# Performance work log

Hardware: AMD Instinct MI355X
Metric: run time of the kernel (lower is better)

## Reference

```python
import jax, jax.numpy as jnp
import numpy as np

NEG_INF = -10000.0  # matches the original max_val init
EPS = 1e-8          # torch.nn.CosineSimilarity default eps


def setup_inputs() -> dict:
    key = jax.random.key(0)
    k1, k2, k3 = jax.random.split(key, 3)
    B, S, H = 32, 1024, 1024
    seq = jax.random.normal(k1, (B, S, H), dtype=jnp.float32)
    # sep0 = index of first [SEP] (end of question), sep1 = end of passage
    sep0 = jax.random.randint(k2, (B, 1), 32, 128)
    sep1 = jax.random.randint(k3, (B, 1), 768, S)
    idxs = jnp.concatenate([sep0, sep1], axis=1).astype(jnp.int64)
    return {"sequence_outputs": seq, "idxs": idxs, "max_ans_len": 32}


def reference(sequence_outputs, idxs, max_ans_len):
    # sequence_outputs: [B, S, H] float; idxs: [B, 2] int (sep0, sep1)
    B, S, H = sequence_outputs.shape
    L = max_ans_len
    sep0 = idxs[:, 0]
    sep1 = idxs[:, 1]

    # question_cat_repr = cat(seq[1], seq[sep0-1]); cos over the 2H concat
    # decomposes as (h_i.q1 + h_j.q2) / (sqrt(|h_i|^2+|h_j|^2) * |q|)
    q1 = sequence_outputs[:, 1, :]                                   # [B, H]
    q2 = jnp.take_along_axis(
        sequence_outputs, (sep0 - 1)[:, None, None], axis=1)[:, 0, :]  # [B, H]
    qn2 = jnp.sum(q1 * q1, -1) + jnp.sum(q2 * q2, -1)                # [B]

    d1 = jnp.einsum('bsh,bh->bs', sequence_outputs, q1)             # [B, S]
    d2 = jnp.einsum('bsh,bh->bs', sequence_outputs, q2)             # [B, S]
    n2 = jnp.sum(sequence_outputs * sequence_outputs, -1)           # [B, S]

    # banded window: for start i, ends j = i + l, l in [0, L)
    i = jnp.arange(S)[:, None]                                      # [S, 1]
    l = jnp.arange(L)[None, :]                                      # [1, L]
    j = jnp.minimum(i + l, S - 1)                                   # [S, L]
    d2w = d2[:, j]                                                  # [B, S, L]
    n2w = n2[:, j]                                                  # [B, S, L]

    denom = jnp.maximum(
        jnp.sqrt((n2[:, :, None] + n2w) * qn2[:, None, None]), EPS)
    sim = (d1[:, :, None] + d2w) / denom                            # [B, S, L]

    # valid ends: j = i + l < min(sep1, i + L); (i+l >= S implies invalid too)
    valid_j = (i + l)[None, :, :] < sep1[:, None, None]
    sim = jnp.where(valid_j, sim, NEG_INF)

    max_vals = jnp.max(sim, axis=-1)                                # [B, S]
    end_idx = jnp.arange(S)[None, :] + jnp.argmax(sim, axis=-1)     # [B, S]

    # valid starts: sep0 + 1 <= i < sep1
    pos = jnp.arange(S)[None, :]
    valid_i = (pos > sep0[:, None]) & (pos < sep1[:, None])
    max_vals = jnp.where(valid_i, max_vals, NEG_INF)
    end_idx = jnp.where(valid_i, end_idx, -1)
    return max_vals, end_idx
```

## Files before the change

kernel.cpp:

```cpp
#include <hip/hip_runtime.h>

#define NEG_INF_F (-10000.0f)
#define EPS_F (1e-8f)

typedef float f4 __attribute__((ext_vector_type(4)));

template <int H>
__global__ __launch_bounds__(256) void row_stats_pipe(
    const float* __restrict__ seq, const int* __restrict__ idxs,
    float* __restrict__ d1, float* __restrict__ d2, float* __restrict__ n2,
    int S, int nrows) {
  constexpr int NF4 = H / 4;
  constexpr int C = H / 256;
  constexpr int R = 4;
  int wave = blockIdx.x * 4 + (threadIdx.x >> 6);
  int lane = threadIdx.x & 63;
  int row0 = wave * R;
  if (row0 >= nrows) return;

  int b = row0 / S;
  int sep0 = idxs[2 * b];

  const f4* base = reinterpret_cast<const f4*>(seq);
  const f4* q1p = base + ((size_t)b * S + 1) * NF4 + lane;
  const f4* q2p = base + ((size_t)b * S + (sep0 - 1)) * NF4 + lane;
  const f4* rp = base + (size_t)row0 * NF4 + lane;

  f4 q1f[C], q2f[C], x[2][C];
  #pragma unroll
  for (int i = 0; i < C; ++i) q1f[i] = q1p[i * 64];
  #pragma unroll
  for (int i = 0; i < C; ++i) q2f[i] = q2p[i * 64];
  #pragma unroll
  for (int i = 0; i < C; ++i) x[0][i] = __builtin_nontemporal_load(rp + i * 64);

  #pragma unroll
  for (int r = 0; r < R; ++r) {
    if (r + 1 < R) {
      const f4* np = rp + (size_t)(r + 1) * NF4;
      #pragma unroll
      for (int i = 0; i < C; ++i)
        x[(r + 1) & 1][i] = __builtin_nontemporal_load(np + i * 64);
    }
    float s1 = 0.f, s2 = 0.f, sn = 0.f;
    #pragma unroll
    for (int i = 0; i < C; ++i) {
      f4 v = x[r & 1][i];
      s1 += v[0] * q1f[i][0] + v[1] * q1f[i][1] + v[2] * q1f[i][2] + v[3] * q1f[i][3];
      s2 += v[0] * q2f[i][0] + v[1] * q2f[i][1] + v[2] * q2f[i][2] + v[3] * q2f[i][3];
      sn += v[0] * v[0] + v[1] * v[1] + v[2] * v[2] + v[3] * v[3];
    }
    #pragma unroll
    for (int off = 32; off >= 1; off >>= 1) {
      s1 += __shfl_xor(s1, off, 64);
      s2 += __shfl_xor(s2, off, 64);
      sn += __shfl_xor(sn, off, 64);
    }
    if (lane == 0) {
      d1[row0 + r] = s1;
      d2[row0 + r] = s2;
      n2[row0 + r] = sn;
    }
  }
}

__global__ __launch_bounds__(256) void row_stats_kernel(
    const float* __restrict__ seq, const int* __restrict__ idxs,
    float* __restrict__ d1, float* __restrict__ d2, float* __restrict__ n2,
    int B, int S, int H) {
  int gtid = blockIdx.x * blockDim.x + threadIdx.x;
  int row = gtid >> 6;
  int lane = threadIdx.x & 63;
  int nrows = B * S;
  if (row >= nrows) return;

  int b = row / S;
  int sep0 = idxs[b * 2 + 0];

  const float* rowp = seq + (size_t)row * H;
  const float* q1p = seq + ((size_t)b * S + 1) * H;
  const float* q2p = seq + ((size_t)b * S + (sep0 - 1)) * H;

  float s1 = 0.f, s2 = 0.f, sn = 0.f;
  for (int h = lane * 4; h < H; h += 64 * 4) {
    float4 x = *reinterpret_cast<const float4*>(rowp + h);
    float4 a = *reinterpret_cast<const float4*>(q1p + h);
    float4 c = *reinterpret_cast<const float4*>(q2p + h);
    s1 += x.x * a.x + x.y * a.y + x.z * a.z + x.w * a.w;
    s2 += x.x * c.x + x.y * c.y + x.z * c.z + x.w * c.w;
    sn += x.x * x.x + x.y * x.y + x.z * x.z + x.w * x.w;
  }
  #pragma unroll
  for (int off = 32; off >= 1; off >>= 1) {
    s1 += __shfl_xor(s1, off, 64);
    s2 += __shfl_xor(s2, off, 64);
    sn += __shfl_xor(sn, off, 64);
  }
  if (lane == 0) {
    d1[row] = s1;
    d2[row] = s2;
    n2[row] = sn;
  }
}

template <int L>
__global__ __launch_bounds__(64) void window_max_fast(
    const float* __restrict__ d1, const float* __restrict__ d2,
    const float* __restrict__ n2, const int* __restrict__ idxs,
    float* __restrict__ out, int S, int nrows) {
  int t = blockIdx.x * 64 + threadIdx.x;
  if (t >= nrows) return;
  int b = t / S;
  int s = t - b * S;

  int sep0 = idxs[b * 2 + 0];
  int sep1 = idxs[b * 2 + 1];

  size_t bS = (size_t)b * S;
  float qn2 = n2[bS + 1] + n2[bS + (sep0 - 1)];
  float my_d1 = d1[t];
  float my_n2 = n2[t];

  const float* d2b = d2 + bS;
  const float* n2b = n2 + bS;

  float best = NEG_INF_F;
  int best_l = 0;
  #pragma unroll
  for (int l = 0; l < L; ++l) {
    int j = min(s + l, S - 1);
    float w2 = n2b[j];
    float v2 = d2b[j];
    float prod = (my_n2 + w2) * qn2;
    float sim = (my_d1 + v2) * __frsqrt_rn(fmaxf(prod, EPS_F * EPS_F));
    sim = (s + l < sep1) ? sim : NEG_INF_F;
    if (sim > best) { best = sim; best_l = l; }
  }

  bool valid_i = (s > sep0) && (s < sep1);
  out[t] = valid_i ? best : NEG_INF_F;
  out[nrows + t] = valid_i ? (float)(s + best_l) : -1.0f;
}

__global__ __launch_bounds__(256) void window_max_kernel(
    const float* __restrict__ d1, const float* __restrict__ d2,
    const float* __restrict__ n2, const int* __restrict__ idxs,
    const int* __restrict__ pL,
    float* __restrict__ out, int B, int S) {
  int t = blockIdx.x * blockDim.x + threadIdx.x;
  int nrows = B * S;
  if (t >= nrows) return;
  int b = t / S;
  int s = t - b * S;

  int sep0 = idxs[b * 2 + 0];
  int sep1 = idxs[b * 2 + 1];
  int L = pL[0];

  float qn2 = n2[(size_t)b * S + 1] + n2[(size_t)b * S + (sep0 - 1)];
  float my_d1 = d1[t];
  float my_n2 = n2[t];

  float best = NEG_INF_F;
  int best_l = 0;
  const float* d2b = d2 + (size_t)b * S;
  const float* n2b = n2 + (size_t)b * S;
  for (int l = 0; l < L; ++l) {
    float sim;
    if (s + l < sep1) {
      int j = min(s + l, S - 1);
      float denom = fmaxf(sqrtf((my_n2 + n2b[j]) * qn2), EPS_F);
      sim = (my_d1 + d2b[j]) / denom;
    } else {
      sim = NEG_INF_F;
    }
    if (sim > best) { best = sim; best_l = l; }
  }

  bool valid_i = (s > sep0) && (s < sep1);
  out[t] = valid_i ? best : NEG_INF_F;
  out[nrows + t] = valid_i ? (float)(s + best_l) : -1.0f;
}

extern "C" void kernel_launch(void* const* d_in, const int* in_sizes, int n_in,
                              void* d_out, int out_size, void* d_ws, size_t ws_size,
                              hipStream_t stream) {
  const float* seq = (const float*)d_in[0];
  const int* idxs = (const int*)d_in[1];
  const int* pL = (const int*)d_in[2];

  int B = in_sizes[1] / 2;
  int S = out_size / (2 * B);
  int H = (int)((long long)in_sizes[0] / ((long long)B * S));
  int nrows = B * S;

  float* d1 = (float*)d_ws;
  float* d2 = d1 + nrows;
  float* n2 = d2 + nrows;

  if (H == 1024 && (S % 4) == 0 && (nrows % 16) == 0) {
    int gridA = nrows / 16;
    row_stats_pipe<1024><<<gridA, 256, 0, stream>>>(seq, idxs, d1, d2, n2, S,
                                                    nrows);
  } else {
    int gridA = (nrows + 3) / 4;
    row_stats_kernel<<<gridA, 256, 0, stream>>>(seq, idxs, d1, d2, n2, B, S, H);
  }

  int gridB = (nrows + 63) / 64;
  window_max_fast<32><<<gridB, 64, 0, stream>>>(d1, d2, n2, idxs,
                                                (float*)d_out, S, nrows);
  (void)pL;
}
```

Before: 31.07 us.

## Parallelize window max across lanes with shuffle argmax reduction

The window-max kernel now gives each window offset its own lane, two start positions per wavefront, and reduces max/argmax with xor shuffles instead of a 32-iteration serial loop per thread. This raises parallelism in the second kernel from 32768 threads to about a million, and each lane loads one neighbor value. In exchange it adds shuffle reduction overhead and redundant per-row loads of idxs and n2. The unused generic window_max_kernel is removed. The first kernel, which reads the 128MB input and likely dominates runtime, is unchanged.

```diff
diff --git a/kernel.cpp b/kernel.cpp
--- a/kernel.cpp
+++ b/kernel.cpp
@@ -104,11 +104,15 @@
 }
 
 template <int L>
-__global__ __launch_bounds__(64) void window_max_fast(
+__global__ __launch_bounds__(256) void window_max_wave(
     const float* __restrict__ d1, const float* __restrict__ d2,
     const float* __restrict__ n2, const int* __restrict__ idxs,
     float* __restrict__ out, int S, int nrows) {
-  int t = blockIdx.x * 64 + threadIdx.x;
+  int wave = blockIdx.x * 4 + (threadIdx.x >> 6);
+  int lane = threadIdx.x & 63;
+  int h = lane >> 5;
+  int l = lane & 31;
+  int t = wave * 2 + h;
   if (t >= nrows) return;
   int b = t / S;
   int s = t - b * S;
@@ -121,65 +125,30 @@
   float my_d1 = d1[t];
   float my_n2 = n2[t];
 
-  const float* d2b = d2 + bS;
-  const float* n2b = n2 + bS;
+  int j = min(s + l, S - 1);
+  float w2 = n2[bS + j];
+  float v2 = d2[bS + j];
+  float prod = (my_n2 + w2) * qn2;
+  float sim = (my_d1 + v2) * __frsqrt_rn(fmaxf(prod, EPS_F * EPS_F));
+  sim = (s + l < sep1) ? sim : NEG_INF_F;
 
-  float best = NEG_INF_F;
-  int best_l = 0;
+  float best = sim;
+  int best_l = l;
   #pragma unroll
-  for (int l = 0; l < L; ++l) {
-    int j = min(s + l, S - 1);
-    float w2 = n2b[j];
-    float v2 = d2b[j];
-    float prod = (my_n2 + w2) * qn2;
-    float sim = (my_d1 + v2) * __frsqrt_rn(fmaxf(prod, EPS_F * EPS_F));
-    sim = (s + l < sep1) ? sim : NEG_INF_F;
-    if (sim > best) { best = sim; best_l = l; }
+  for (int off = 16; off >= 1; off >>= 1) {
+    float ov = __shfl_xor(best, off, 64);
+    int oi = __shfl_xor(best_l, off, 64);
+    if (ov > best || (ov == best && oi < best_l)) {
+      best = ov;
+      best_l = oi;
+    }
   }
 
-  bool valid_i = (s > sep0) && (s < sep1);
-  out[t] = valid_i ? best : NEG_INF_F;
-  out[nrows + t] = valid_i ? (float)(s + best_l) : -1.0f;
-}
-
-__global__ __launch_bounds__(256) void window_max_kernel(
-    const float* __restrict__ d1, const float* __restrict__ d2,
-    const float* __restrict__ n2, const int* __restrict__ idxs,
-    const int* __restrict__ pL,
-    float* __restrict__ out, int B, int S) {
-  int t = blockIdx.x * blockDim.x + threadIdx.x;
-  int nrows = B * S;
-  if (t >= nrows) return;
-  int b = t / S;
-  int s = t - b * S;
-
-  int sep0 = idxs[b * 2 + 0];
-  int sep1 = idxs[b * 2 + 1];
-  int L = pL[0];
-
-  float qn2 = n2[(size_t)b * S + 1] + n2[(size_t)b * S + (sep0 - 1)];
-  float my_d1 = d1[t];
-  float my_n2 = n2[t];
-
-  float best = NEG_INF_F;
-  int best_l = 0;
-  const float* d2b = d2 + (size_t)b * S;
-  const float* n2b = n2 + (size_t)b * S;
-  for (int l = 0; l < L; ++l) {
-    float sim;
-    if (s + l < sep1) {
-      int j = min(s + l, S - 1);
-      float denom = fmaxf(sqrtf((my_n2 + n2b[j]) * qn2), EPS_F);
-      sim = (my_d1 + d2b[j]) / denom;
-    } else {
-      sim = NEG_INF_F;
-    }
-    if (sim > best) { best = sim; best_l = l; }
+  if (l == 0) {
+    bool valid_i = (s > sep0) && (s < sep1);
+    out[t] = valid_i ? best : NEG_INF_F;
+    out[nrows + t] = valid_i ? (float)(s + best_l) : -1.0f;
   }
-
-  bool valid_i = (s > sep0) && (s < sep1);
-  out[t] = valid_i ? best : NEG_INF_F;
-  out[nrows + t] = valid_i ? (float)(s + best_l) : -1.0f;
 }
 
 extern "C" void kernel_launch(void* const* d_in, const int* in_sizes, int n_in,
@@ -207,8 +176,8 @@
     row_stats_kernel<<<gridA, 256, 0, stream>>>(seq, idxs, d1, d2, n2, B, S, H);
   }
 
-  int gridB = (nrows + 63) / 64;
-  window_max_fast<32><<<gridB, 64, 0, stream>>>(d1, d2, n2, idxs,
-                                                (float*)d_out, S, nrows);
+  int gridB = (nrows + 7) / 8;
+  window_max_wave<32><<<gridB, 256, 0, stream>>>(d1, d2, n2, idxs,
+                                                 (float*)d_out, S, nrows);
   (void)pL;
 }
```

Result: slower. 31.99 us (+2.9%).
